# Performance work log

Hardware: AMD Instinct MI355X
Metric: run time of the kernel (lower is better)

The kernel has to match this reference:

```python
import jax, jax.numpy as jnp
import numpy as np

B, L, DM = 8, 1024, 1024
H, P, N, K = 32, 64, 128, 4   # nheads, headdim, d_state, d_conv
DI = H * P                    # d_inner = expand * d_model = 2048
DXBC = DI + 2 * N             # conv channels = 2304
DINP = 2 * DI + 2 * N + H     # in_proj width = 4404
ED = 2048                     # embed_dim

def setup_inputs():
    key = jax.random.key(0)
    ks = jax.random.split(key, 10)
    s = lambda i, shape, scale=0.02: jax.random.normal(ks[i], shape, jnp.float32) * scale
    return {
        "bert_out": jax.random.normal(ks[0], (B, L, 1024), jnp.float32),
        "w_pb": s(1, (1024, DM)), "b_pb": jnp.zeros((DM,), jnp.float32),
        "w_in": s(2, (DM, DINP)),
        "conv_w": s(3, (DXBC, K), 0.2), "conv_b": jnp.zeros((DXBC,), jnp.float32),
        "dt_bias": jax.random.uniform(ks[4], (H,), jnp.float32, -4.0, 0.0),
        "A_log": jnp.log(jnp.arange(1, H + 1, dtype=jnp.float32)),
        "D": jnp.ones((H,), jnp.float32),
        "norm_w": jnp.ones((DI,), jnp.float32),
        "w_outp": s(5, (DI, DM)),
        "w_attn": s(6, (DM, 1)), "b_attn": jnp.zeros((1,), jnp.float32),
        "w_emb": s(7, (DM, ED)), "b_emb": jnp.zeros((ED,), jnp.float32),
    }

def reference(bert_out, w_pb, b_pb, w_in, conv_w, conv_b, dt_bias, A_log, D,
              norm_w, w_outp, w_attn, b_attn, w_emb, b_emb):
    x = bert_out @ w_pb + b_pb                          # [B,L,DM] proj_bert
    # ---- Mamba2 ----
    zxbcdt = x @ w_in                                   # [B,L,DINP]
    z, xBC, dt = jnp.split(zxbcdt, [DI, DI + DXBC], axis=-1)
    # causal depthwise conv1d (kernel K) + SiLU
    xp = jnp.pad(xBC, ((0, 0), (K - 1, 0), (0, 0)))
    xBC = sum(xp[:, k:k + L, :] * conv_w[:, k] for k in range(K)) + conv_b
    xBC = jax.nn.silu(xBC)
    xs, Bm, Cm = jnp.split(xBC, [DI, DI + N], axis=-1)  # [B,L,DI],[B,L,N],[B,L,N]
    xs = xs.reshape(B, L, H, P)
    dt = jax.nn.softplus(dt + dt_bias)                  # [B,L,H]
    dA = jnp.exp(dt * (-jnp.exp(A_log)))                # [B,L,H]
    def step(h, inp):
        dA_t, dt_t, B_t, C_t, x_t = inp
        h = h * dA_t[:, :, None, None] + jnp.einsum('bh,bn,bhp->bhpn', dt_t, B_t, x_t)
        return h, jnp.einsum('bhpn,bn->bhp', h, C_t)
    h0 = jnp.zeros((B, H, P, N), x.dtype)
    _, ys = jax.lax.scan(step, h0, (dA.transpose(1, 0, 2), dt.transpose(1, 0, 2),
                                    Bm.transpose(1, 0, 2), Cm.transpose(1, 0, 2),
                                    xs.transpose(1, 0, 2, 3)))
    y = ys.transpose(1, 0, 2, 3) + D[None, None, :, None] * xs   # skip term
    y = y.reshape(B, L, DI) * jax.nn.silu(z)                     # gated
    y = y * jax.lax.rsqrt(jnp.mean(y * y, axis=-1, keepdims=True) + 1e-5) * norm_w
    emb = y @ w_outp                                             # [B,L,DM]
    # ---- attention pooling ----
    w = jax.nn.softmax(emb @ w_attn + b_attn, axis=1)            # [B,L,1]
    pooled = (emb * w).sum(axis=1)                               # [B,DM]
    # dropout is identity in eval mode
    return pooled @ w_emb + b_emb                                # [B,ED]
```

## Files before the change

kernel.cpp:

```cpp
#include <hip/hip_runtime.h>
#include <hip/hip_bf16.h>
#include <math.h>

#define B_    8
#define L_    1024
#define DM_   1024
#define H_    32
#define P_    64
#define NS_   128
#define DI_   2048
#define DXBC_ 2304
#define DINP_ 4384
#define ED_   2048

typedef __attribute__((ext_vector_type(8))) short bf8_t;
typedef __attribute__((ext_vector_type(8))) unsigned short u16x8;
typedef __attribute__((ext_vector_type(4))) float f4_t;

__device__ __forceinline__ float silu_f(float x) { return x / (1.f + __expf(-x)); }

__device__ __forceinline__ unsigned short f2bf(float x) {
    unsigned u = __float_as_uint(x);
    unsigned r = u + 0x7fffu + ((u >> 16) & 1u);
    return (unsigned short)(r >> 16);
}
__device__ __forceinline__ float bf2f(unsigned short h) {
    return __uint_as_float(((unsigned)h) << 16);
}

__global__ __launch_bounds__(256) void convw_k(
    const float* __restrict__ W, unsigned short* __restrict__ hi,
    unsigned short* __restrict__ lo, int K, int N, int Npad)
{
    size_t e = (size_t)blockIdx.x * 256 + threadIdx.x;
    if (e >= (size_t)K * Npad) return;
    int n = (int)(e % Npad), k = (int)(e / Npad);
    float v = (n < N) ? W[(size_t)k * N + n] : 0.f;
    unsigned short h = f2bf(v);
    unsigned short l = f2bf(v - bf2f(h));
    int nt = n >> 7, r = n & 127, kt = k >> 5, c = k & 31;
    size_t dst = ((size_t)(nt * (K >> 5) + kt) << 12) + (r << 5) + c;
    hi[dst] = h; lo[dst] = l;
}

template<bool CHECK_N>
__global__ __launch_bounds__(256, 2) void bgemm_k(
    const float* __restrict__ A, const unsigned short* __restrict__ Whi,
    const unsigned short* __restrict__ Wlo, float* __restrict__ C,
    const float* __restrict__ bias, int M, int N, int K, int ldc)
{
    __shared__ unsigned short Ah[128 * 40], Al[128 * 40];
    __shared__ unsigned short Bh[128 * 40], Bl[128 * 40];
    const int tid = threadIdx.x;
    const int m0 = blockIdx.y * 128, n0 = blockIdx.x * 128;
    const int lane = tid & 63;
    const int wv = tid >> 6;
    const int wr = wv >> 1, wc = wv & 1;
    const int l15 = lane & 15, l4 = lane >> 4;
    const int KT = K >> 5;

    f4_t acc[4][4];
#pragma unroll
    for (int i = 0; i < 4; i++)
#pragma unroll
        for (int j = 0; j < 4; j++) acc[i][j] = (f4_t){0.f, 0.f, 0.f, 0.f};

    const int ar = tid >> 2;
    const int ac = (tid & 3) * 8;
    const int wrow = tid >> 1;
    const int wcol = (tid & 1) * 16;

    for (int kt = 0; kt < KT; ++kt) {
        const int k0 = kt * 32;
        const float* Ap0 = A + (size_t)(m0 + ar) * K + k0 + ac;
        const float* Ap1 = Ap0 + (size_t)64 * K;
        float4 a00 = *(const float4*)Ap0, a01 = *(const float4*)(Ap0 + 4);
        float4 a10 = *(const float4*)Ap1, a11 = *(const float4*)(Ap1 + 4);
        const unsigned short* Whp = Whi + (((size_t)(blockIdx.x * KT + kt)) << 12);
        const unsigned short* Wlp = Wlo + (((size_t)(blockIdx.x * KT + kt)) << 12);
        u16x8 whv0 = *(const u16x8*)(Whp + (wrow << 5) + wcol);
        u16x8 whv1 = *(const u16x8*)(Whp + (wrow << 5) + wcol + 8);
        u16x8 wlv0 = *(const u16x8*)(Wlp + (wrow << 5) + wcol);
        u16x8 wlv1 = *(const u16x8*)(Wlp + (wrow << 5) + wcol + 8);

        __syncthreads();
        {
            float av0[8] = {a00.x, a00.y, a00.z, a00.w, a01.x, a01.y, a01.z, a01.w};
            float av1[8] = {a10.x, a10.y, a10.z, a10.w, a11.x, a11.y, a11.z, a11.w};
            u16x8 vh0, vl0, vh1, vl1;
#pragma unroll
            for (int j = 0; j < 8; j++) {
                unsigned short h0 = f2bf(av0[j]);
                vh0[j] = h0; vl0[j] = f2bf(av0[j] - bf2f(h0));
                unsigned short h1 = f2bf(av1[j]);
                vh1[j] = h1; vl1[j] = f2bf(av1[j] - bf2f(h1));
            }
            *(u16x8*)&Ah[ar * 40 + ac] = vh0;
            *(u16x8*)&Al[ar * 40 + ac] = vl0;
            *(u16x8*)&Ah[(ar + 64) * 40 + ac] = vh1;
            *(u16x8*)&Al[(ar + 64) * 40 + ac] = vl1;
            *(u16x8*)&Bh[wrow * 40 + wcol]     = whv0;
            *(u16x8*)&Bh[wrow * 40 + wcol + 8] = whv1;
            *(u16x8*)&Bl[wrow * 40 + wcol]     = wlv0;
            *(u16x8*)&Bl[wrow * 40 + wcol + 8] = wlv1;
        }
        __syncthreads();

        bf8_t afh[4], afl[4], bfh[4], bfl[4];
#pragma unroll
        for (int i = 0; i < 4; i++) {
            int off = (wr * 64 + i * 16 + l15) * 40 + l4 * 8;
            afh[i] = *(const bf8_t*)&Ah[off];
            afl[i] = *(const bf8_t*)&Al[off];
        }
#pragma unroll
        for (int j = 0; j < 4; j++) {
            int off = (wc * 64 + j * 16 + l15) * 40 + l4 * 8;
            bfh[j] = *(const bf8_t*)&Bh[off];
            bfl[j] = *(const bf8_t*)&Bl[off];
        }
#pragma unroll
        for (int i = 0; i < 4; i++)
#pragma unroll
            for (int j = 0; j < 4; j++) {
                acc[i][j] = __builtin_amdgcn_mfma_f32_16x16x32_bf16(afh[i], bfh[j], acc[i][j], 0, 0, 0);
                acc[i][j] = __builtin_amdgcn_mfma_f32_16x16x32_bf16(afl[i], bfh[j], acc[i][j], 0, 0, 0);
                acc[i][j] = __builtin_amdgcn_mfma_f32_16x16x32_bf16(afh[i], bfl[j], acc[i][j], 0, 0, 0);
            }
    }

#pragma unroll
    for (int j = 0; j < 4; j++) {
        int col = n0 + wc * 64 + j * 16 + l15;
        bool ok = !CHECK_N || (col < N);
        float bv = 0.f;
        if (bias && ok) bv = bias[col];
        if (ok) {
#pragma unroll
            for (int i = 0; i < 4; i++) {
                int rbase = m0 + wr * 64 + i * 16 + l4 * 4;
#pragma unroll
                for (int r = 0; r < 4; r++)
                    C[(size_t)(rbase + r) * ldc + col] = acc[i][j][r] + bv;
            }
        }
    }
}

template<bool CHECK_N>
__global__ __launch_bounds__(256, 2) void sgemm_k(
    const float* __restrict__ A, const float* __restrict__ Bw,
    float* __restrict__ C, const float* __restrict__ bias,
    int M, int N, int K, int ldb, int ldc)
{
    __shared__ float As[16][128];
    __shared__ float Bs[16][128];
    const int tid = threadIdx.x;
    const int m0 = blockIdx.y * 128;
    const int n0 = blockIdx.x * 128;
    const int tx = tid & 15;
    const int ty = tid >> 4;
    const int arr = tid >> 1;
    const int acc_ = (tid & 1) * 8;
    const int bk = tid >> 5;
    const int bn = (tid & 31) * 4;

    float acc[8][8];
#pragma unroll
    for (int i = 0; i < 8; i++)
#pragma unroll
        for (int j = 0; j < 8; j++) acc[i][j] = 0.f;

    for (int k0 = 0; k0 < K; k0 += 16) {
        float4 a0 = *(const float4*)(A + (size_t)(m0 + arr) * K + k0 + acc_);
        float4 a1 = *(const float4*)(A + (size_t)(m0 + arr) * K + k0 + acc_ + 4);
        float4 b0, b1;
        if (!CHECK_N || (n0 + bn) < N) {
            b0 = *(const float4*)(Bw + (size_t)(k0 + bk) * ldb + n0 + bn);
            b1 = *(const float4*)(Bw + (size_t)(k0 + bk + 8) * ldb + n0 + bn);
        } else {
            b0 = make_float4(0.f, 0.f, 0.f, 0.f);
            b1 = make_float4(0.f, 0.f, 0.f, 0.f);
        }
        __syncthreads();
        As[acc_ + 0][arr] = a0.x; As[acc_ + 1][arr] = a0.y;
        As[acc_ + 2][arr] = a0.z; As[acc_ + 3][arr] = a0.w;
        As[acc_ + 4][arr] = a1.x; As[acc_ + 5][arr] = a1.y;
        As[acc_ + 6][arr] = a1.z; As[acc_ + 7][arr] = a1.w;
        *(float4*)&Bs[bk][bn]     = b0;
        *(float4*)&Bs[bk + 8][bn] = b1;
        __syncthreads();
#pragma unroll
        for (int kk = 0; kk < 16; kk++) {
            float4 av0 = *(const float4*)&As[kk][ty * 8];
            float4 av1 = *(const float4*)&As[kk][ty * 8 + 4];
            float4 bv0 = *(const float4*)&Bs[kk][tx * 4];
            float4 bv1 = *(const float4*)&Bs[kk][64 + tx * 4];
            float a_[8] = {av0.x, av0.y, av0.z, av0.w, av1.x, av1.y, av1.z, av1.w};
            float b_[8] = {bv0.x, bv0.y, bv0.z, bv0.w, bv1.x, bv1.y, bv1.z, bv1.w};
#pragma unroll
            for (int i = 0; i < 8; i++)
#pragma unroll
                for (int j = 0; j < 8; j++) acc[i][j] += a_[i] * b_[j];
        }
    }
    float4 bb0 = make_float4(0.f, 0.f, 0.f, 0.f), bb1 = bb0;
    if (bias) {
        if (!CHECK_N || (n0 + tx * 4) < N)      bb0 = *(const float4*)(bias + n0 + tx * 4);
        if (!CHECK_N || (n0 + 64 + tx * 4) < N) bb1 = *(const float4*)(bias + n0 + 64 + tx * 4);
    }
#pragma unroll
    for (int i = 0; i < 8; i++) {
        size_t row = (size_t)(m0 + ty * 8 + i) * ldc + n0;
        if (!CHECK_N || (n0 + tx * 4) < N) {
            float4 v = make_float4(acc[i][0] + bb0.x, acc[i][1] + bb0.y,
                                   acc[i][2] + bb0.z, acc[i][3] + bb0.w);
            *(float4*)(C + row + tx * 4) = v;
        }
        if (!CHECK_N || (n0 + 64 + tx * 4) < N) {
            float4 v = make_float4(acc[i][4] + bb1.x, acc[i][5] + bb1.y,
                                   acc[i][6] + bb1.z, acc[i][7] + bb1.w);
            *(float4*)(C + row + 64 + tx * 4) = v;
        }
    }
}

__global__ __launch_bounds__(256) void dt_k(
    const float* __restrict__ zx, const float* __restrict__ dt_bias,
    const float* __restrict__ A_log, float* __restrict__ dtp, float* __restrict__ dAb)
{
    int e = blockIdx.x * 256 + threadIdx.x;
    int l = e & 1023;
    int h = (e >> 10) & 31;
    int b = e >> 15;
    float dtr = zx[((size_t)b * L_ + l) * DINP_ + (DI_ + DXBC_) + h];
    float u = dtr + dt_bias[h];
    float sp = (u > 20.f) ? u : log1pf(__expf(u));
    float da = __expf(-__expf(A_log[h]) * sp);
    size_t o = ((size_t)b * H_ + h) * L_ + l;
    dtp[o] = sp;
    dAb[o] = da;
}

__global__ __launch_bounds__(256) void stash_k(const float* __restrict__ zx, float* __restrict__ stash)
{
    int e = blockIdx.x * 256 + threadIdx.x;
    int c = e % DXBC_;
    int r = e / DXBC_;
    int k = r % 3;
    int bc = r / 3;
    int chunk = bc & 7;
    int b = bc >> 3;
    int t = chunk * 128 - 3 + k;
    float v = 0.f;
    if (t >= 0) v = zx[((size_t)b * L_ + t) * DINP_ + DI_ + c];
    stash[e] = v;
}

__global__ __launch_bounds__(256) void conv_k(
    float* __restrict__ zx, const float* __restrict__ cw,
    const float* __restrict__ cb, const float* __restrict__ stash)
{
    int tid = threadIdx.x;
    int cblk = blockIdx.x;
    int chunk = blockIdx.y;
    int b = blockIdx.z;
    int c = cblk * 256 + tid;
    float4 w = *(const float4*)(cw + (size_t)c * 4);
    float bias = cb[c];
    const float* st = stash + ((size_t)(b * 8 + chunk) * 3) * DXBC_ + c;
    float x0 = st[0], x1 = st[DXBC_], x2 = st[2 * DXBC_];
    int t0 = chunk * 128;
    size_t base = ((size_t)b * L_ + t0) * DINP_ + DI_ + c;
#pragma unroll 4
    for (int t = 0; t < 128; t++) {
        float xt = zx[base + (size_t)t * DINP_];
        float a = w.x * x0 + w.y * x1 + w.z * x2 + w.w * xt + bias;
        a = a / (1.f + __expf(-a));
        zx[base + (size_t)t * DINP_] = a;
        x0 = x1; x1 = x2; x2 = xt;
    }
}

__global__ __launch_bounds__(1024, 1) void scan_k(
    const float* __restrict__ zx, const float* __restrict__ dtp,
    const float* __restrict__ dAb, const float* __restrict__ Dp,
    float* __restrict__ ys)
{
    int bh = blockIdx.x;
    int b = bh >> 5, h = bh & 31;
    int tid = threadIdx.x;
    int lane = tid & 63;
    int gu = __builtin_amdgcn_readfirstlane(tid >> 6);
    int nbase = gu * 8;
    __shared__ float ypart[8][16][64];
    __shared__ float bcs[8][256];
    __shared__ float xss[8][64];
    __shared__ float dtda[2][8];
    float hreg[8];
#pragma unroll
    for (int j = 0; j < 8; j++) hreg[j] = 0.f;
    float Dh = Dp[h];
    const float* dtrow = dtp + ((size_t)b * H_ + h) * L_;
    const float* darow = dAb + ((size_t)b * H_ + h) * L_;

    const int st_t = tid >> 7;
    const int st_j = (tid & 127) * 2;
    const int sx_t = tid >> 6;
    const int sx_ok = (sx_t < 8);

    {
        size_t row = ((size_t)b * L_ + st_t) * DINP_;
        float2 bc2 = *(const float2*)(zx + row + 2 * DI_ + st_j);
        *(float2*)&bcs[st_t][st_j] = bc2;
        if (sx_ok) {
            size_t rowx = ((size_t)b * L_ + sx_t) * DINP_;
            xss[sx_t][lane] = zx[rowx + DI_ + h * 64 + lane];
        }
        if (tid < 8)               dtda[0][tid] = dtrow[tid];
        else if (tid < 16)         dtda[1][tid - 8] = darow[tid - 8];
    }
    __syncthreads();

    float xout = 0.f;
    for (int c0 = 0; c0 < L_; c0 += 8) {
        float2 nbc; float nx = 0.f, nd = 0.f;
        const bool pf = (c0 + 8) < L_;
        if (pf) {
            size_t row = ((size_t)b * L_ + c0 + 8 + st_t) * DINP_;
            nbc = *(const float2*)(zx + row + 2 * DI_ + st_j);
            if (sx_ok) {
                size_t rowx = ((size_t)b * L_ + c0 + 8 + sx_t) * DINP_;
                nx = zx[rowx + DI_ + h * 64 + lane];
            }
            if (tid < 8)       nd = dtrow[c0 + 8 + tid];
            else if (tid < 16) nd = darow[c0 + 8 + tid - 8];
        }
#pragma unroll
        for (int tt = 0; tt < 8; ++tt) {
            float dtv = dtda[0][tt];
            float dav = dtda[1][tt];
            float xv  = xss[tt][lane];
            if (tt == gu) xout = xv;
            float4 b0  = *(const float4*)&bcs[tt][nbase];
            float4 b1  = *(const float4*)&bcs[tt][nbase + 4];
            float4 cv0 = *(const float4*)&bcs[tt][128 + nbase];
            float4 cv1 = *(const float4*)&bcs[tt][128 + nbase + 4];
            float u = dtv * xv;
            float ya = 0.f, yb = 0.f;
            hreg[0] = hreg[0] * dav + u * b0.x; ya += hreg[0] * cv0.x;
            hreg[1] = hreg[1] * dav + u * b0.y; yb += hreg[1] * cv0.y;
            hreg[2] = hreg[2] * dav + u * b0.z; ya += hreg[2] * cv0.z;
            hreg[3] = hreg[3] * dav + u * b0.w; yb += hreg[3] * cv0.w;
            hreg[4] = hreg[4] * dav + u * b1.x; ya += hreg[4] * cv1.x;
            hreg[5] = hreg[5] * dav + u * b1.y; yb += hreg[5] * cv1.y;
            hreg[6] = hreg[6] * dav + u * b1.z; ya += hreg[6] * cv1.z;
            hreg[7] = hreg[7] * dav + u * b1.w; yb += hreg[7] * cv1.w;
            ypart[tt][gu][lane] = ya + yb;
        }
        __syncthreads();
        if (gu < 8) {
            int t = c0 + gu;
            float v = 0.f;
#pragma unroll
            for (int w = 0; w < 16; w++) v += ypart[gu][w][lane];
            ys[((size_t)b * L_ + t) * DI_ + h * 64 + lane] = v + Dh * xout;
        }
        if (pf) {
            *(float2*)&bcs[st_t][st_j] = nbc;
            if (sx_ok) xss[sx_t][lane] = nx;
            if (tid < 8)       dtda[0][tid] = nd;
            else if (tid < 16) dtda[1][tid - 8] = nd;
        }
        __syncthreads();
    }
}

__global__ __launch_bounds__(256) void gate_norm_k(
    float* __restrict__ ys, const float* __restrict__ zx, const float* __restrict__ nw)
{
    int row = blockIdx.x;
    int tid = threadIdx.x;
    float* yr = ys + (size_t)row * DI_;
    const float* zr = zx + (size_t)row * DINP_;
    float4 v[2];
    float ss = 0.f;
#pragma unroll
    for (int i = 0; i < 2; i++) {
        int d = tid * 4 + i * 1024;
        float4 yv = *(const float4*)(yr + d);
        float4 zv = *(const float4*)(zr + d);
        v[i].x = yv.x * silu_f(zv.x);
        v[i].y = yv.y * silu_f(zv.y);
        v[i].z = yv.z * silu_f(zv.z);
        v[i].w = yv.w * silu_f(zv.w);
        ss += v[i].x * v[i].x + v[i].y * v[i].y + v[i].z * v[i].z + v[i].w * v[i].w;
    }
    __shared__ float red[256];
    red[tid] = ss;
    __syncthreads();
    for (int s = 128; s > 0; s >>= 1) {
        if (tid < s) red[tid] += red[tid + s];
        __syncthreads();
    }
    float scale = rsqrtf(red[0] / (float)DI_ + 1e-5f);
#pragma unroll
    for (int i = 0; i < 2; i++) {
        int d = tid * 4 + i * 1024;
        float4 nwv = *(const float4*)(nw + d);
        float4 o = make_float4(v[i].x * scale * nwv.x, v[i].y * scale * nwv.y,
                               v[i].z * scale * nwv.z, v[i].w * scale * nwv.w);
        *(float4*)(yr + d) = o;
    }
}

__global__ __launch_bounds__(256) void attnw_k(
    const float* __restrict__ emb, const float* __restrict__ wat,
    const float* __restrict__ batn, float* __restrict__ logits)
{
    int row = blockIdx.x * 4 + (threadIdx.x >> 6);
    int lane = threadIdx.x & 63;
    const float* er = emb + (size_t)row * DM_;
    float s = 0.f;
#pragma unroll
    for (int k = 0; k < 16; k++) s += er[lane + k * 64] * wat[lane + k * 64];
#pragma unroll
    for (int off = 32; off; off >>= 1) s += __shfl_down(s, off);
    if (lane == 0) logits[row] = s + batn[0];
}

__global__ __launch_bounds__(256) void softmax_k(
    const float* __restrict__ logits, float* __restrict__ wght, float* __restrict__ pooled)
{
    int b = blockIdx.x;
    int tid = threadIdx.x;
    __shared__ float red[256];
    float4 lv = *(const float4*)(logits + (size_t)b * L_ + tid * 4);
    float m = fmaxf(fmaxf(lv.x, lv.y), fmaxf(lv.z, lv.w));
    red[tid] = m;
    __syncthreads();
    for (int s = 128; s > 0; s >>= 1) {
        if (tid < s) red[tid] = fmaxf(red[tid], red[tid + s]);
        __syncthreads();
    }
    float bm = red[0];
    __syncthreads();
    float e0 = __expf(lv.x - bm), e1 = __expf(lv.y - bm);
    float e2 = __expf(lv.z - bm), e3 = __expf(lv.w - bm);
    red[tid] = e0 + e1 + e2 + e3;
    __syncthreads();
    for (int s = 128; s > 0; s >>= 1) {
        if (tid < s) red[tid] += red[tid + s];
        __syncthreads();
    }
    float inv = 1.f / red[0];
    *(float4*)(wght + (size_t)b * L_ + tid * 4) = make_float4(e0 * inv, e1 * inv, e2 * inv, e3 * inv);
    *(float4*)(pooled + (size_t)b * DM_ + tid * 4) = make_float4(0.f, 0.f, 0.f, 0.f);
}

__global__ __launch_bounds__(256) void pool_k(
    const float* __restrict__ emb, const float* __restrict__ wght, float* __restrict__ pooled)
{
    int b = blockIdx.x, dc = blockIdx.y, lc = blockIdx.z;
    int d = dc * 256 + threadIdx.x;
    const float* wr = wght + (size_t)b * L_ + lc * 64;
    float acc = 0.f;
#pragma unroll 4
    for (int lt = 0; lt < 64; lt++)
        acc += emb[((size_t)(b * L_ + lc * 64 + lt)) * DM_ + d] * wr[lt];
    atomicAdd(pooled + (size_t)b * DM_ + d, acc);
}

__global__ __launch_bounds__(256) void outp_k(
    const float* __restrict__ pooled, const float* __restrict__ wemb,
    const float* __restrict__ bemb, float* __restrict__ out)
{
    int ec = blockIdx.x, b = blockIdx.y;
    int tid = threadIdx.x;
    __shared__ float pl[DM_];
#pragma unroll
    for (int i = 0; i < 4; i++) pl[tid + i * 256] = pooled[(size_t)b * DM_ + tid + i * 256];
    __syncthreads();
    int e = ec * 256 + tid;
    float acc = bemb[e];
#pragma unroll 4
    for (int d = 0; d < DM_; d++) acc += pl[d] * wemb[(size_t)d * ED_ + e];
    out[(size_t)b * ED_ + e] = acc;
}

extern "C" void kernel_launch(void* const* d_in, const int* in_sizes, int n_in,
                              void* d_out, int out_size, void* d_ws, size_t ws_size,
                              hipStream_t stream)
{
    (void)in_sizes; (void)n_in; (void)out_size;
    const float* bert    = (const float*)d_in[0];
    const float* w_pb    = (const float*)d_in[1];
    const float* b_pb    = (const float*)d_in[2];
    const float* w_in    = (const float*)d_in[3];
    const float* conv_w  = (const float*)d_in[4];
    const float* conv_b  = (const float*)d_in[5];
    const float* dt_bias = (const float*)d_in[6];
    const float* A_log   = (const float*)d_in[7];
    const float* Dp      = (const float*)d_in[8];
    const float* norm_w  = (const float*)d_in[9];
    const float* w_outp  = (const float*)d_in[10];
    const float* w_attn  = (const float*)d_in[11];
    const float* b_attn  = (const float*)d_in[12];
    const float* w_emb   = (const float*)d_in[13];
    const float* b_emb   = (const float*)d_in[14];
    float* out = (float*)d_out;

    float* ws     = (float*)d_ws;
    float* zx     = ws;
    float* ys     = zx  + (size_t)8192 * 4384;
    float* xe     = ys  + (size_t)8192 * 2048;
    float* dtp    = xe  + (size_t)8192 * 1024;
    float* dAb    = dtp + 262144;
    float* stash  = dAb + 262144;
    float* logits = stash + 442368;
    float* wght   = logits + 8192;
    float* pooled = wght + 8192;
    float* fend   = pooled + 8192;

    size_t wpb_n = (size_t)8  * 32 * 4096;
    size_t win_n = (size_t)35 * 32 * 4096;
    size_t wop_n = (size_t)8  * 64 * 4096;
    unsigned short* wpb_h = (unsigned short*)ys;
    unsigned short* wpb_l = wpb_h + wpb_n;
    unsigned short* win_h = wpb_l + wpb_n;
    unsigned short* win_l = win_h + win_n;
    unsigned short* wop_h = (unsigned short*)zx;
    unsigned short* wop_l = wop_h + wop_n;

    size_t need_bytes = (size_t)((char*)fend - (char*)d_ws);
    bool use_mfma = ws_size >= need_bytes;

    if (use_mfma) {
        convw_k<<<(unsigned)(((size_t)1024 * 1024 + 255) / 256), 256, 0, stream>>>(
            w_pb, wpb_h, wpb_l, 1024, 1024, 1024);
        convw_k<<<(unsigned)(((size_t)1024 * 4480 + 255) / 256), 256, 0, stream>>>(
            w_in, win_h, win_l, 1024, 4384, 4480);
        bgemm_k<false><<<dim3(8, 64), 256, 0, stream>>>(bert, wpb_h, wpb_l, xe, b_pb,
                                                        8192, 1024, 1024, 1024);
        bgemm_k<true><<<dim3(35, 64), 256, 0, stream>>>(xe, win_h, win_l, zx, nullptr,
                                                        8192, 4384, 1024, 4384);
    } else {
        sgemm_k<false><<<dim3(8, 64), 256, 0, stream>>>(bert, w_pb, xe, b_pb,
                                                        8192, 1024, 1024, 1024, 1024);
        sgemm_k<true><<<dim3(35, 64), 256, 0, stream>>>(xe, w_in, zx, nullptr,
                                                        8192, 4384, 1024, 4384, 4384);
    }
    dt_k<<<1024, 256, 0, stream>>>(zx, dt_bias, A_log, dtp, dAb);
    stash_k<<<1728, 256, 0, stream>>>(zx, stash);
    conv_k<<<dim3(9, 8, 8), 256, 0, stream>>>(zx, conv_w, conv_b, stash);
    scan_k<<<256, 1024, 0, stream>>>(zx, dtp, dAb, Dp, ys);
    gate_norm_k<<<8192, 256, 0, stream>>>(ys, zx, norm_w);
    if (use_mfma) {
        convw_k<<<(unsigned)(((size_t)2048 * 1024 + 255) / 256), 256, 0, stream>>>(
            w_outp, wop_h, wop_l, 2048, 1024, 1024);
        bgemm_k<false><<<dim3(8, 64), 256, 0, stream>>>(ys, wop_h, wop_l, xe, nullptr,
                                                        8192, 1024, 2048, 1024);
    } else {
        sgemm_k<false><<<dim3(8, 64), 256, 0, stream>>>(ys, w_outp, xe, nullptr,
                                                        8192, 1024, 2048, 1024, 1024);
    }
    attnw_k<<<2048, 256, 0, stream>>>(xe, w_attn, b_attn, logits);
    softmax_k<<<8, 256, 0, stream>>>(logits, wght, pooled);
    pool_k<<<dim3(8, 4, 16), 256, 0, stream>>>(xe, wght, pooled);
    outp_k<<<dim3(8, 8), 256, 0, stream>>>(pooled, w_emb, b_emb, out);
}
```

Measured before the change: 975.1 us.

## Pre-split activations into tiled bf16 hi/lo buffers and prefetch next k-tile

```diff
diff --git a/kernel.cpp b/kernel.cpp
--- a/kernel.cpp
+++ b/kernel.cpp
@@ -43,11 +43,26 @@
     hi[dst] = h; lo[dst] = l;
 }
 
+__global__ __launch_bounds__(256) void conva_k(
+    const float* __restrict__ A, unsigned short* __restrict__ hi,
+    unsigned short* __restrict__ lo, int M, int K)
+{
+    size_t e = (size_t)blockIdx.x * 256 + threadIdx.x;
+    if (e >= (size_t)M * K) return;
+    int k = (int)(e % K), m = (int)(e / K);
+    float v = A[e];
+    unsigned short h = f2bf(v);
+    unsigned short l = f2bf(v - bf2f(h));
+    int mt = m >> 7, r = m & 127, kt = k >> 5, c = k & 31;
+    size_t dst = ((size_t)(mt * (K >> 5) + kt) << 12) + (r << 5) + c;
+    hi[dst] = h; lo[dst] = l;
+}
+
 template<bool CHECK_N>
 __global__ __launch_bounds__(256, 2) void bgemm_k(
-    const float* __restrict__ A, const unsigned short* __restrict__ Whi,
-    const unsigned short* __restrict__ Wlo, float* __restrict__ C,
-    const float* __restrict__ bias, int M, int N, int K, int ldc)
+    const unsigned short* __restrict__ Ahi, const unsigned short* __restrict__ Alo,
+    const unsigned short* __restrict__ Whi, const unsigned short* __restrict__ Wlo,
+    float* __restrict__ C, const float* __restrict__ bias, int N, int K, int ldc)
 {
     __shared__ unsigned short Ah[128 * 40], Al[128 * 40];
     __shared__ unsigned short Bh[128 * 40], Bl[128 * 40];
@@ -65,46 +80,32 @@
 #pragma unroll
         for (int j = 0; j < 4; j++) acc[i][j] = (f4_t){0.f, 0.f, 0.f, 0.f};
 
-    const int ar = tid >> 2;
-    const int ac = (tid & 3) * 8;
-    const int wrow = tid >> 1;
-    const int wcol = (tid & 1) * 16;
-
+    const int trow = tid >> 1;
+    const int tcol = (tid & 1) * 16;
+    const int soff = trow * 40 + tcol;
+
+    u16x8 rAh0, rAh1, rAl0, rAl1, rWh0, rWh1, rWl0, rWl1;
+#define LOADKT(KTI) {                                                               \
+        size_t aoff = (((size_t)(blockIdx.y * KT + (KTI))) << 12) + (trow << 5) + tcol; \
+        size_t woff = (((size_t)(blockIdx.x * KT + (KTI))) << 12) + (trow << 5) + tcol; \
+        rAh0 = *(const u16x8*)(Ahi + aoff); rAh1 = *(const u16x8*)(Ahi + aoff + 8); \
+        rAl0 = *(const u16x8*)(Alo + aoff); rAl1 = *(const u16x8*)(Alo + aoff + 8); \
+        rWh0 = *(const u16x8*)(Whi + woff); rWh1 = *(const u16x8*)(Whi + woff + 8); \
+        rWl0 = *(const u16x8*)(Wlo + woff); rWl1 = *(const u16x8*)(Wlo + woff + 8); }
+
+    LOADKT(0);
     for (int kt = 0; kt < KT; ++kt) {
-        const int k0 = kt * 32;
-        const float* Ap0 = A + (size_t)(m0 + ar) * K + k0 + ac;
-        const float* Ap1 = Ap0 + (size_t)64 * K;
-        float4 a00 = *(const float4*)Ap0, a01 = *(const float4*)(Ap0 + 4);
-        float4 a10 = *(const float4*)Ap1, a11 = *(const float4*)(Ap1 + 4);
-        const unsigned short* Whp = Whi + (((size_t)(blockIdx.x * KT + kt)) << 12);
-        const unsigned short* Wlp = Wlo + (((size_t)(blockIdx.x * KT + kt)) << 12);
-        u16x8 whv0 = *(const u16x8*)(Whp + (wrow << 5) + wcol);
-        u16x8 whv1 = *(const u16x8*)(Whp + (wrow << 5) + wcol + 8);
-        u16x8 wlv0 = *(const u16x8*)(Wlp + (wrow << 5) + wcol);
-        u16x8 wlv1 = *(const u16x8*)(Wlp + (wrow << 5) + wcol + 8);
-
-        __syncthreads();
-        {
-            float av0[8] = {a00.x, a00.y, a00.z, a00.w, a01.x, a01.y, a01.z, a01.w};
-            float av1[8] = {a10.x, a10.y, a10.z, a10.w, a11.x, a11.y, a11.z, a11.w};
-            u16x8 vh0, vl0, vh1, vl1;
-#pragma unroll
-            for (int j = 0; j < 8; j++) {
-                unsigned short h0 = f2bf(av0[j]);
-                vh0[j] = h0; vl0[j] = f2bf(av0[j] - bf2f(h0));
-                unsigned short h1 = f2bf(av1[j]);
-                vh1[j] = h1; vl1[j] = f2bf(av1[j] - bf2f(h1));
-            }
-            *(u16x8*)&Ah[ar * 40 + ac] = vh0;
-            *(u16x8*)&Al[ar * 40 + ac] = vl0;
-            *(u16x8*)&Ah[(ar + 64) * 40 + ac] = vh1;
-            *(u16x8*)&Al[(ar + 64) * 40 + ac] = vl1;
-            *(u16x8*)&Bh[wrow * 40 + wcol]     = whv0;
-            *(u16x8*)&Bh[wrow * 40 + wcol + 8] = whv1;
-            *(u16x8*)&Bl[wrow * 40 + wcol]     = wlv0;
-            *(u16x8*)&Bl[wrow * 40 + wcol + 8] = wlv1;
-        }
-        __syncthreads();
+        __syncthreads();
+        *(u16x8*)&Ah[soff]     = rAh0;
+        *(u16x8*)&Ah[soff + 8] = rAh1;
+        *(u16x8*)&Al[soff]     = rAl0;
+        *(u16x8*)&Al[soff + 8] = rAl1;
+        *(u16x8*)&Bh[soff]     = rWh0;
+        *(u16x8*)&Bh[soff + 8] = rWh1;
+        *(u16x8*)&Bl[soff]     = rWl0;
+        *(u16x8*)&Bl[soff + 8] = rWl1;
+        __syncthreads();
+        if (kt + 1 < KT) LOADKT(kt + 1);
 
         bf8_t afh[4], afl[4], bfh[4], bfl[4];
 #pragma unroll
@@ -128,6 +129,7 @@
                 acc[i][j] = __builtin_amdgcn_mfma_f32_16x16x32_bf16(afh[i], bfl[j], acc[i][j], 0, 0, 0);
             }
     }
+#undef LOADKT
 
 #pragma unroll
     for (int j = 0; j < 4; j++) {
@@ -525,12 +527,18 @@
     size_t wpb_n = (size_t)8  * 32 * 4096;
     size_t win_n = (size_t)35 * 32 * 4096;
     size_t wop_n = (size_t)8  * 64 * 4096;
+    size_t aT_n  = (size_t)64 * 32 * 4096;
+    size_t ysT_n = (size_t)64 * 64 * 4096;
     unsigned short* wpb_h = (unsigned short*)ys;
     unsigned short* wpb_l = wpb_h + wpb_n;
     unsigned short* win_h = wpb_l + wpb_n;
     unsigned short* win_l = win_h + win_n;
+    unsigned short* aT_h  = win_l + win_n;
+    unsigned short* aT_l  = aT_h + aT_n;
     unsigned short* wop_h = (unsigned short*)zx;
     unsigned short* wop_l = wop_h + wop_n;
+    unsigned short* ysT_h = (unsigned short*)zx + 6291456;
+    unsigned short* ysT_l = ysT_h + ysT_n;
 
     size_t need_bytes = (size_t)((char*)fend - (char*)d_ws);
     bool use_mfma = ws_size >= need_bytes;
@@ -540,10 +548,12 @@
             w_pb, wpb_h, wpb_l, 1024, 1024, 1024);
         convw_k<<<(unsigned)(((size_t)1024 * 4480 + 255) / 256), 256, 0, stream>>>(
             w_in, win_h, win_l, 1024, 4384, 4480);
-        bgemm_k<false><<<dim3(8, 64), 256, 0, stream>>>(bert, wpb_h, wpb_l, xe, b_pb,
-                                                        8192, 1024, 1024, 1024);
-        bgemm_k<true><<<dim3(35, 64), 256, 0, stream>>>(xe, win_h, win_l, zx, nullptr,
-                                                        8192, 4384, 1024, 4384);
+        conva_k<<<32768, 256, 0, stream>>>(bert, aT_h, aT_l, 8192, 1024);
+        bgemm_k<false><<<dim3(8, 64), 256, 0, stream>>>(aT_h, aT_l, wpb_h, wpb_l,
+                                                        xe, b_pb, 1024, 1024, 1024);
+        conva_k<<<32768, 256, 0, stream>>>(xe, aT_h, aT_l, 8192, 1024);
+        bgemm_k<true><<<dim3(35, 64), 256, 0, stream>>>(aT_h, aT_l, win_h, win_l,
+                                                        zx, nullptr, 4384, 1024, 4384);
     } else {
         sgemm_k<false><<<dim3(8, 64), 256, 0, stream>>>(bert, w_pb, xe, b_pb,
                                                         8192, 1024, 1024, 1024, 1024);
@@ -558,8 +568,9 @@
     if (use_mfma) {
         convw_k<<<(unsigned)(((size_t)2048 * 1024 + 255) / 256), 256, 0, stream>>>(
             w_outp, wop_h, wop_l, 2048, 1024, 1024);
-        bgemm_k<false><<<dim3(8, 64), 256, 0, stream>>>(ys, wop_h, wop_l, xe, nullptr,
-                                                        8192, 1024, 2048, 1024);
+        conva_k<<<65536, 256, 0, stream>>>(ys, ysT_h, ysT_l, 8192, 2048);
+        bgemm_k<false><<<dim3(8, 64), 256, 0, stream>>>(ysT_h, ysT_l, wop_h, wop_l,
+                                                        xe, nullptr, 1024, 2048, 1024);
     } else {
         sgemm_k<false><<<dim3(8, 64), 256, 0, stream>>>(ys, w_outp, xe, nullptr,
                                                         8192, 1024, 2048, 1024, 1024);
```

Result: slower. 1.022 ms (+4.8%).

## Replace sequential selective scan with chunked SSD scan on MFMA

Applied to the files above, without the earlier changes.

```diff
diff --git a/kernel.cpp b/kernel.cpp
--- a/kernel.cpp
+++ b/kernel.cpp
@@ -15,6 +15,7 @@
 
 typedef __attribute__((ext_vector_type(8))) short bf8_t;
 typedef __attribute__((ext_vector_type(8))) unsigned short u16x8;
+typedef __attribute__((ext_vector_type(4))) unsigned short u16x4;
 typedef __attribute__((ext_vector_type(4))) float f4_t;
 
 __device__ __forceinline__ float silu_f(float x) { return x / (1.f + __expf(-x)); }
@@ -143,84 +144,6 @@
                 for (int r = 0; r < 4; r++)
                     C[(size_t)(rbase + r) * ldc + col] = acc[i][j][r] + bv;
             }
-        }
-    }
-}
-
-template<bool CHECK_N>
-__global__ __launch_bounds__(256, 2) void sgemm_k(
-    const float* __restrict__ A, const float* __restrict__ Bw,
-    float* __restrict__ C, const float* __restrict__ bias,
-    int M, int N, int K, int ldb, int ldc)
-{
-    __shared__ float As[16][128];
-    __shared__ float Bs[16][128];
-    const int tid = threadIdx.x;
-    const int m0 = blockIdx.y * 128;
-    const int n0 = blockIdx.x * 128;
-    const int tx = tid & 15;
-    const int ty = tid >> 4;
-    const int arr = tid >> 1;
-    const int acc_ = (tid & 1) * 8;
-    const int bk = tid >> 5;
-    const int bn = (tid & 31) * 4;
-
-    float acc[8][8];
-#pragma unroll
-    for (int i = 0; i < 8; i++)
-#pragma unroll
-        for (int j = 0; j < 8; j++) acc[i][j] = 0.f;
-
-    for (int k0 = 0; k0 < K; k0 += 16) {
-        float4 a0 = *(const float4*)(A + (size_t)(m0 + arr) * K + k0 + acc_);
-        float4 a1 = *(const float4*)(A + (size_t)(m0 + arr) * K + k0 + acc_ + 4);
-        float4 b0, b1;
-        if (!CHECK_N || (n0 + bn) < N) {
-            b0 = *(const float4*)(Bw + (size_t)(k0 + bk) * ldb + n0 + bn);
-            b1 = *(const float4*)(Bw + (size_t)(k0 + bk + 8) * ldb + n0 + bn);
-        } else {
-            b0 = make_float4(0.f, 0.f, 0.f, 0.f);
-            b1 = make_float4(0.f, 0.f, 0.f, 0.f);
-        }
-        __syncthreads();
-        As[acc_ + 0][arr] = a0.x; As[acc_ + 1][arr] = a0.y;
-        As[acc_ + 2][arr] = a0.z; As[acc_ + 3][arr] = a0.w;
-        As[acc_ + 4][arr] = a1.x; As[acc_ + 5][arr] = a1.y;
-        As[acc_ + 6][arr] = a1.z; As[acc_ + 7][arr] = a1.w;
-        *(float4*)&Bs[bk][bn]     = b0;
-        *(float4*)&Bs[bk + 8][bn] = b1;
-        __syncthreads();
-#pragma unroll
-        for (int kk = 0; kk < 16; kk++) {
-            float4 av0 = *(const float4*)&As[kk][ty * 8];
-            float4 av1 = *(const float4*)&As[kk][ty * 8 + 4];
-            float4 bv0 = *(const float4*)&Bs[kk][tx * 4];
-            float4 bv1 = *(const float4*)&Bs[kk][64 + tx * 4];
-            float a_[8] = {av0.x, av0.y, av0.z, av0.w, av1.x, av1.y, av1.z, av1.w};
-            float b_[8] = {bv0.x, bv0.y, bv0.z, bv0.w, bv1.x, bv1.y, bv1.z, bv1.w};
-#pragma unroll
-            for (int i = 0; i < 8; i++)
-#pragma unroll
-                for (int j = 0; j < 8; j++) acc[i][j] += a_[i] * b_[j];
-        }
-    }
-    float4 bb0 = make_float4(0.f, 0.f, 0.f, 0.f), bb1 = bb0;
-    if (bias) {
-        if (!CHECK_N || (n0 + tx * 4) < N)      bb0 = *(const float4*)(bias + n0 + tx * 4);
-        if (!CHECK_N || (n0 + 64 + tx * 4) < N) bb1 = *(const float4*)(bias + n0 + 64 + tx * 4);
-    }
-#pragma unroll
-    for (int i = 0; i < 8; i++) {
-        size_t row = (size_t)(m0 + ty * 8 + i) * ldc + n0;
-        if (!CHECK_N || (n0 + tx * 4) < N) {
-            float4 v = make_float4(acc[i][0] + bb0.x, acc[i][1] + bb0.y,
-                                   acc[i][2] + bb0.z, acc[i][3] + bb0.w);
-            *(float4*)(C + row + tx * 4) = v;
-        }
-        if (!CHECK_N || (n0 + 64 + tx * 4) < N) {
-            float4 v = make_float4(acc[i][4] + bb1.x, acc[i][5] + bb1.y,
-                                   acc[i][6] + bb1.z, acc[i][7] + bb1.w);
-            *(float4*)(C + row + 64 + tx * 4) = v;
         }
     }
 }
@@ -376,6 +299,215 @@
     }
 }
 
+__global__ __launch_bounds__(512, 1) void scan_c_k(
+    const float* __restrict__ zx, const float* __restrict__ dtp,
+    const float* __restrict__ dAb, const float* __restrict__ Dp,
+    float* __restrict__ ys)
+{
+    const int bh = blockIdx.x;
+    const int b = bh >> 5, h = bh & 31;
+    const int tid = threadIdx.x;
+    const int lane = tid & 63;
+    const int wv = tid >> 6;
+    const int l15 = lane & 15, l4 = lane >> 4;
+
+    __shared__ unsigned short BbH[8192], BbL[8192];
+    __shared__ unsigned short CbH[8192], CbL[8192];
+    __shared__ unsigned short XTH[4608], XTL[4608];
+    __shared__ unsigned short BtH[9216], BtL[9216];
+    __shared__ float hT[8448];
+    __shared__ float cls[64], dtc[64];
+
+    const float Dh = Dp[h];
+    const float* dtrow = dtp + ((size_t)b * H_ + h) * L_;
+    const float* darow = dAb + ((size_t)b * H_ + h) * L_;
+
+    for (int i = tid; i < 8448; i += 512) hT[i] = 0.f;
+    __syncthreads();
+
+    for (int c = 0; c < 16; ++c) {
+        const int t0 = c * 64;
+#pragma unroll
+        for (int it = 0; it < 8; ++it) {
+            int flat = (it * 512 + tid) * 4;
+            int row = flat >> 8, j = flat & 255;
+            float4 v = *(const float4*)(zx + ((size_t)(b * L_) + t0 + row) * DINP_ + 2 * DI_ + j);
+            float vv[4] = {v.x, v.y, v.z, v.w};
+            u16x4 vh, vl;
+#pragma unroll
+            for (int e = 0; e < 4; e++) {
+                unsigned short hh = f2bf(vv[e]);
+                vh[e] = hh; vl[e] = f2bf(vv[e] - bf2f(hh));
+            }
+            int sw = (row & 7) << 3;
+            if (j < 128) {
+                int idx = row * 128 + (j ^ sw);
+                *(u16x4*)&BbH[idx] = vh; *(u16x4*)&BbL[idx] = vl;
+            } else {
+                int idx = row * 128 + ((j - 128) ^ sw);
+                *(u16x4*)&CbH[idx] = vh; *(u16x4*)&CbL[idx] = vl;
+            }
+        }
+#pragma unroll
+        for (int it = 0; it < 8; ++it) {
+            int flat = it * 512 + tid;
+            int row = flat >> 6, p = flat & 63;
+            float v = zx[((size_t)(b * L_) + t0 + row) * DINP_ + DI_ + h * 64 + p];
+            unsigned short hh = f2bf(v), ll = f2bf(v - bf2f(hh));
+            int ix = p * 72 + (row ^ ((p & 7) << 3));
+            XTH[ix] = hh; XTL[ix] = ll;
+        }
+        if (tid < 64) {
+            float la = __logf(darow[t0 + lane]);
+#pragma unroll
+            for (int d = 1; d < 64; d <<= 1) {
+                float o = __shfl_up(la, d, 64);
+                if (lane >= d) la += o;
+            }
+            cls[lane] = la;
+        } else if (tid < 128) {
+            dtc[lane] = dtrow[t0 + lane];
+        }
+        __syncthreads();
+
+        {
+            int si = wv >> 1;
+#pragma unroll
+            for (int jj = 0; jj < 2; ++jj) {
+                int tj = (wv & 1) * 2 + jj;
+                f4_t g = (f4_t){0.f, 0.f, 0.f, 0.f};
+#pragma unroll
+                for (int kf = 0; kf < 4; ++kf) {
+                    int rowA = si * 16 + l15, kb = kf * 32 + l4 * 8;
+                    int ia = rowA * 128 + (kb ^ ((rowA & 7) << 3));
+                    bf8_t ah = *(const bf8_t*)&BbH[ia];
+                    bf8_t al = *(const bf8_t*)&BbL[ia];
+                    int rowB = tj * 16 + l15;
+                    int ib = rowB * 128 + (kb ^ ((rowB & 7) << 3));
+                    bf8_t bh = *(const bf8_t*)&CbH[ib];
+                    bf8_t bl = *(const bf8_t*)&CbL[ib];
+                    g = __builtin_amdgcn_mfma_f32_16x16x32_bf16(ah, bh, g, 0, 0, 0);
+                    g = __builtin_amdgcn_mfma_f32_16x16x32_bf16(al, bh, g, 0, 0, 0);
+                    g = __builtin_amdgcn_mfma_f32_16x16x32_bf16(ah, bl, g, 0, 0, 0);
+                }
+#pragma unroll
+                for (int r = 0; r < 4; ++r) {
+                    int s_idx = si * 16 + l4 * 4 + r;
+                    int t_idx = tj * 16 + l15;
+                    float val = 0.f;
+                    if (s_idx <= t_idx)
+                        val = __expf(cls[t_idx] - cls[s_idx]) * dtc[s_idx] * g[r];
+                    unsigned short hh = f2bf(val), ll = f2bf(val - bf2f(hh));
+                    int im = t_idx * 72 + (s_idx ^ ((t_idx & 7) << 3));
+                    BtH[im] = hh; BtL[im] = ll;
+                }
+            }
+        }
+        __syncthreads();
+
+        {
+            int ti = wv >> 1;
+#pragma unroll
+            for (int jj = 0; jj < 2; ++jj) {
+                int pj = (wv & 1) * 2 + jj;
+                f4_t aI = (f4_t){0.f, 0.f, 0.f, 0.f};
+                f4_t aN = (f4_t){0.f, 0.f, 0.f, 0.f};
+#pragma unroll
+                for (int kf = 0; kf < 2; ++kf) {
+                    int rowA = ti * 16 + l15, kb = kf * 32 + l4 * 8;
+                    int ia = rowA * 72 + (kb ^ ((rowA & 7) << 3));
+                    bf8_t mh = *(const bf8_t*)&BtH[ia];
+                    bf8_t ml = *(const bf8_t*)&BtL[ia];
+                    int rowP = pj * 16 + l15;
+                    int ip = rowP * 72 + (kb ^ ((rowP & 7) << 3));
+                    bf8_t xh = *(const bf8_t*)&XTH[ip];
+                    bf8_t xl = *(const bf8_t*)&XTL[ip];
+                    aI = __builtin_amdgcn_mfma_f32_16x16x32_bf16(mh, xh, aI, 0, 0, 0);
+                    aI = __builtin_amdgcn_mfma_f32_16x16x32_bf16(ml, xh, aI, 0, 0, 0);
+                    aI = __builtin_amdgcn_mfma_f32_16x16x32_bf16(mh, xl, aI, 0, 0, 0);
+                }
+#pragma unroll
+                for (int kf = 0; kf < 4; ++kf) {
+                    int rowA = ti * 16 + l15, kb = kf * 32 + l4 * 8;
+                    int ia = rowA * 128 + (kb ^ ((rowA & 7) << 3));
+                    bf8_t ch = *(const bf8_t*)&CbH[ia];
+                    bf8_t cl_ = *(const bf8_t*)&CbL[ia];
+                    int rowP = pj * 16 + l15;
+                    const float* hp = &hT[rowP * 132 + kb];
+                    float4 h0 = *(const float4*)hp, h1 = *(const float4*)(hp + 4);
+                    float hv[8] = {h0.x, h0.y, h0.z, h0.w, h1.x, h1.y, h1.z, h1.w};
+                    bf8_t hh, hl;
+#pragma unroll
+                    for (int e = 0; e < 8; e++) {
+                        unsigned short q = f2bf(hv[e]);
+                        hh[e] = (short)q; hl[e] = (short)f2bf(hv[e] - bf2f(q));
+                    }
+                    aN = __builtin_amdgcn_mfma_f32_16x16x32_bf16(ch, hh, aN, 0, 0, 0);
+                    aN = __builtin_amdgcn_mfma_f32_16x16x32_bf16(cl_, hh, aN, 0, 0, 0);
+                    aN = __builtin_amdgcn_mfma_f32_16x16x32_bf16(ch, hl, aN, 0, 0, 0);
+                }
+#pragma unroll
+                for (int r = 0; r < 4; ++r) {
+                    int t_idx = ti * 16 + l4 * 4 + r;
+                    int p_idx = pj * 16 + l15;
+                    int ix = p_idx * 72 + (t_idx ^ ((p_idx & 7) << 3));
+                    float xv = bf2f(XTH[ix]) + bf2f(XTL[ix]);
+                    float yv = aI[r] + __expf(cls[t_idx]) * aN[r] + Dh * xv;
+                    ys[((size_t)(b * L_) + t0 + t_idx) * DI_ + h * 64 + p_idx] = yv;
+                }
+            }
+        }
+        __syncthreads();
+
+        {
+            float cls63 = cls[63];
+#pragma unroll
+            for (int it = 0; it < 16; ++it) {
+                int flat = it * 512 + tid;
+                int s = flat >> 7, n = flat & 127;
+                int ib = s * 128 + (n ^ ((s & 7) << 3));
+                float bvv = bf2f(BbH[ib]) + bf2f(BbL[ib]);
+                float w = __expf(cls63 - cls[s]) * dtc[s] * bvv;
+                unsigned short hh = f2bf(w), ll = f2bf(w - bf2f(hh));
+                int io = n * 72 + (s ^ ((n & 7) << 3));
+                BtH[io] = hh; BtL[io] = ll;
+            }
+        }
+        __syncthreads();
+
+        {
+            float dl = __expf(cls[63]);
+            int nt = wv;
+#pragma unroll
+            for (int pj = 0; pj < 4; ++pj) {
+                f4_t a = (f4_t){0.f, 0.f, 0.f, 0.f};
+#pragma unroll
+                for (int kf = 0; kf < 2; ++kf) {
+                    int rowA = nt * 16 + l15, kb = kf * 32 + l4 * 8;
+                    int ia = rowA * 72 + (kb ^ ((rowA & 7) << 3));
+                    bf8_t th = *(const bf8_t*)&BtH[ia];
+                    bf8_t tl = *(const bf8_t*)&BtL[ia];
+                    int rowP = pj * 16 + l15;
+                    int ip = rowP * 72 + (kb ^ ((rowP & 7) << 3));
+                    bf8_t xh = *(const bf8_t*)&XTH[ip];
+                    bf8_t xl = *(const bf8_t*)&XTL[ip];
+                    a = __builtin_amdgcn_mfma_f32_16x16x32_bf16(th, xh, a, 0, 0, 0);
+                    a = __builtin_amdgcn_mfma_f32_16x16x32_bf16(tl, xh, a, 0, 0, 0);
+                    a = __builtin_amdgcn_mfma_f32_16x16x32_bf16(th, xl, a, 0, 0, 0);
+                }
+#pragma unroll
+                for (int r = 0; r < 4; ++r) {
+                    int n_idx = nt * 16 + l4 * 4 + r;
+                    int p_idx = pj * 16 + l15;
+                    int ih = p_idx * 132 + n_idx;
+                    hT[ih] = dl * hT[ih] + a[r];
+                }
+            }
+        }
+        __syncthreads();
+    }
+}
+
 __global__ __launch_bounds__(256) void gate_norm_k(
     float* __restrict__ ys, const float* __restrict__ zx, const float* __restrict__ nw)
 {
@@ -545,24 +677,21 @@
         bgemm_k<true><<<dim3(35, 64), 256, 0, stream>>>(xe, win_h, win_l, zx, nullptr,
                                                         8192, 4384, 1024, 4384);
     } else {
-        sgemm_k<false><<<dim3(8, 64), 256, 0, stream>>>(bert, w_pb, xe, b_pb,
-                                                        8192, 1024, 1024, 1024, 1024);
-        sgemm_k<true><<<dim3(35, 64), 256, 0, stream>>>(xe, w_in, zx, nullptr,
-                                                        8192, 4384, 1024, 4384, 4384);
+        bgemm_k<false><<<dim3(8, 64), 256, 0, stream>>>(bert, wpb_h, wpb_l, xe, b_pb,
+                                                        8192, 1024, 1024, 1024);
+        bgemm_k<true><<<dim3(35, 64), 256, 0, stream>>>(xe, win_h, win_l, zx, nullptr,
+                                                        8192, 4384, 1024, 4384);
     }
     dt_k<<<1024, 256, 0, stream>>>(zx, dt_bias, A_log, dtp, dAb);
     stash_k<<<1728, 256, 0, stream>>>(zx, stash);
     conv_k<<<dim3(9, 8, 8), 256, 0, stream>>>(zx, conv_w, conv_b, stash);
-    scan_k<<<256, 1024, 0, stream>>>(zx, dtp, dAb, Dp, ys);
+    scan_c_k<<<256, 512, 0, stream>>>(zx, dtp, dAb, Dp, ys);
     gate_norm_k<<<8192, 256, 0, stream>>>(ys, zx, norm_w);
-    if (use_mfma) {
+    {
         convw_k<<<(unsigned)(((size_t)2048 * 1024 + 255) / 256), 256, 0, stream>>>(
             w_outp, wop_h, wop_l, 2048, 1024, 1024);
         bgemm_k<false><<<dim3(8, 64), 256, 0, stream>>>(ys, wop_h, wop_l, xe, nullptr,
                                                         8192, 1024, 2048, 1024);
-    } else {
-        sgemm_k<false><<<dim3(8, 64), 256, 0, stream>>>(ys, w_outp, xe, nullptr,
-                                                        8192, 1024, 2048, 1024, 1024);
     }
     attnw_k<<<2048, 256, 0, stream>>>(xe, w_attn, b_attn, logits);
     softmax_k<<<8, 256, 0, stream>>>(logits, wght, pooled);
```

Measured after the change: 1.274 ms. +30.6%, slower.
